# Optimization experiments

Hardware: AMD Instinct MI355X
Metric: run time of the kernel (lower is better)

The kernel has to match this reference:

```python
import jax, jax.numpy as jnp
import numpy as np

N = 50000      # total nodes in batch
E = 600000     # total edges
F_IN = 128     # num_features
H = 128        # nhid
C = 10         # num_classes
G = 100        # number of graphs in batch
RATIO = 0.5    # pooling_ratio


def _glorot(k, shape):
    lim = (6.0 / (shape[0] + shape[1])) ** 0.5
    return jax.random.uniform(k, shape, minval=-lim, maxval=lim, dtype=jnp.float32)


def setup_inputs() -> dict:
    key = jax.random.key(0)
    ks = jax.random.split(key, 20)
    inp = {
        "x": jax.random.normal(ks[0], (N, F_IN), dtype=jnp.float32),
        "edge_index": jax.random.randint(ks[1], (2, E), 0, N),
        "batch": jnp.sort(jax.random.randint(ks[2], (N,), 0, G)),
        # conv1/pool1
        "W1": _glorot(ks[3], (F_IN, H)), "b1": jnp.zeros((H,), jnp.float32),
        "Ws1": _glorot(ks[4], (H, 1)), "bs1": jnp.zeros((1,), jnp.float32),
        # conv2/pool2
        "W2": _glorot(ks[5], (H, H)), "b2": jnp.zeros((H,), jnp.float32),
        "Ws2": _glorot(ks[6], (H, 1)), "bs2": jnp.zeros((1,), jnp.float32),
        # conv3/pool3
        "W3": _glorot(ks[7], (H, H)), "b3": jnp.zeros((H,), jnp.float32),
        "Ws3": _glorot(ks[8], (H, 1)), "bs3": jnp.zeros((1,), jnp.float32),
        # MLP head
        "Wl1": _glorot(ks[9], (2 * H, H)), "bl1": jnp.zeros((H,), jnp.float32),
        "Wl2": _glorot(ks[10], (H, H // 2)), "bl2": jnp.zeros((H // 2,), jnp.float32),
        "Wl3": _glorot(ks[11], (H // 2, C)), "bl3": jnp.zeros((C,), jnp.float32),
    }
    return inp


def _gcn_conv(x, W, b, src, dst, ew):
    # PyG GCNConv: D^{-1/2}(A+I)D^{-1/2} X W + b, with masked edge weights ew.
    xw = x @ W                                                  # [N, out]
    deg = jax.ops.segment_sum(ew, dst, num_segments=N) + 1.0    # self-loop
    norm = jax.lax.rsqrt(deg)
    coef = norm[src] * norm[dst] * ew                           # [E]
    agg = jax.ops.segment_sum(xw[src] * coef[:, None], dst, num_segments=N)
    return agg + xw * (norm * norm)[:, None] + b


def _topk_mask(score, node_mask, batch, ratio):
    # Per-graph top-ceil(ratio * active) selection, expressed as a node mask.
    score_m = jnp.where(node_mask > 0, score, -jnp.inf)
    active = jax.ops.segment_sum(node_mask, batch, num_segments=G)
    k = jnp.ceil(ratio * active)
    order = jnp.argsort(-score_m)                         # score desc
    perm = order[jnp.argsort(batch[order], stable=True)]  # batch asc, score desc
    total = jax.ops.segment_sum(jnp.ones((N,), score.dtype), batch, num_segments=G)
    starts = jnp.cumsum(total) - total
    b_sorted = batch[perm]
    rank = jnp.arange(N, dtype=score.dtype) - starts[b_sorted]
    keep_sorted = rank < k[b_sorted]
    keep = jnp.zeros((N,), bool).at[perm].set(keep_sorted)
    return node_mask * keep.astype(node_mask.dtype)


def _readout(x, node_mask, batch):
    # [gmp | gap] per graph, honoring the active-node mask.
    m = node_mask[:, None]
    s = jax.ops.segment_sum(x * m, batch, num_segments=G)
    cnt = jax.ops.segment_sum(node_mask, batch, num_segments=G)
    mean = s / jnp.maximum(cnt, 1.0)[:, None]
    xm = jnp.where(m > 0, x, -jnp.inf)
    mx = jax.ops.segment_max(xm, batch, num_segments=G)
    mx = jnp.where(jnp.isfinite(mx), mx, 0.0)
    return jnp.concatenate([mx, mean], axis=1)            # [G, 2H]


def reference(x, edge_index, batch, W1, b1, Ws1, bs1, W2, b2, Ws2, bs2,
              W3, b3, Ws3, bs3, Wl1, bl1, Wl2, bl2, Wl3, bl3):
    src, dst = edge_index[0], edge_index[1]

    def block(h, mask, W, b, Ws, bs):
        ew = mask[src] * mask[dst]
        h = jax.nn.relu(_gcn_conv(h, W, b, src, dst, ew))
        score = _gcn_conv(h, Ws, bs, src, dst, ew)[:, 0]
        new_mask = _topk_mask(score, mask, batch, RATIO)
        h = h * jnp.tanh(score)[:, None] * new_mask[:, None]
        return h, new_mask

    mask = jnp.ones((N,), jnp.float32)
    h, mask = block(x, mask, W1, b1, Ws1, bs1)
    r1 = _readout(h, mask, batch)
    h, mask = block(h, mask, W2, b2, Ws2, bs2)
    r2 = _readout(h, mask, batch)
    h, mask = block(h, mask, W3, b3, Ws3, bs3)
    r3 = _readout(h, mask, batch)

    z = r1 + r2 + r3                                       # [G, 2H]
    z = jax.nn.relu(z @ Wl1 + bl1)                         # dropout is eval-mode no-op
    z = jax.nn.relu(z @ Wl2 + bl2)
    return jax.nn.log_softmax(z @ Wl3 + bl3, axis=-1)      # [G, C]
```

## Files before the change

### kernel.cpp

```cpp
#include <hip/hip_runtime.h>
#include <math.h>

#define N_NODES 50000
#define N_EDGES 600000
#define H 128
#define G_GRAPHS 100
#define C_CLS 10
#define NBLK_SCAN ((N_NODES + 255) / 256)
#define RSUB 16


__global__ void fill_kernel(float* __restrict__ p, float v, int n) {
    int i = blockIdx.x * 256 + threadIdx.x;
    if (i < n) p[i] = v;
}

__global__ void starts_kernel(const int* __restrict__ batch, int* __restrict__ starts, int n) {
    int i = blockIdx.x * 256 + threadIdx.x;
    if (i >= n) return;
    int b = batch[i];
    int prev = (i == 0) ? -1 : batch[i - 1];
    for (int g = prev + 1; g <= b; ++g) starts[g] = i;
    if (i == n - 1) {
        for (int g = b + 1; g < G_GRAPHS; ++g) starts[g] = n;
    }
}

__global__ void counts_kernel(const int* __restrict__ starts, int* __restrict__ counts) {
    int g = threadIdx.x;
    if (g < G_GRAPHS) {
        int e = (g == G_GRAPHS - 1) ? N_NODES : starts[g + 1];
        counts[g] = e - starts[g];
    }
}


__global__ void indeg_kernel(const int* __restrict__ dst, int* __restrict__ indeg, int ne) {
    int e = blockIdx.x * 256 + threadIdx.x;
    if (e < ne) atomicAdd(&indeg[dst[e]], 1);
}

__global__ void bsum_kernel(const int* __restrict__ indeg, int* __restrict__ bsum, int n) {
    __shared__ int red[256];
    int i = blockIdx.x * 256 + threadIdx.x;
    red[threadIdx.x] = (i < n) ? indeg[i] : 0;
    __syncthreads();
    for (int o = 128; o > 0; o >>= 1) {
        if (threadIdx.x < o) red[threadIdx.x] += red[threadIdx.x + o];
        __syncthreads();
    }
    if (threadIdx.x == 0) bsum[blockIdx.x] = red[0];
}

__global__ void bscan_kernel(const int* __restrict__ bsum, int* __restrict__ boff, int nb) {
    __shared__ int s[256];
    int t = threadIdx.x;
    s[t] = (t < nb) ? bsum[t] : 0;
    __syncthreads();
    for (int o = 1; o < 256; o <<= 1) {
        int v = (t >= o) ? s[t - o] : 0;
        __syncthreads();
        s[t] += v;
        __syncthreads();
    }
    if (t < nb) boff[t] = (t == 0) ? 0 : s[t - 1];
}

__global__ void rowptr_kernel(const int* __restrict__ indeg, const int* __restrict__ boff,
                              int* __restrict__ rowptr, int n) {
    __shared__ int s[256];
    int i = blockIdx.x * 256 + threadIdx.x;
    int t = threadIdx.x;
    int v = (i < n) ? indeg[i] : 0;
    s[t] = v;
    __syncthreads();
    for (int o = 1; o < 256; o <<= 1) {
        int u = (t >= o) ? s[t - o] : 0;
        __syncthreads();
        s[t] += u;
        __syncthreads();
    }
    int incl = s[t];
    int excl = incl - v;
    if (i < n) rowptr[i] = boff[blockIdx.x] + excl;
    if (i == n - 1) rowptr[n] = boff[blockIdx.x] + incl;
}

__global__ void scatter_kernel(const int* __restrict__ src, const int* __restrict__ dst,
                               const int* __restrict__ rowptr, int* __restrict__ cursor,
                               int* __restrict__ srcC, int ne) {
    int e = blockIdx.x * 256 + threadIdx.x;
    if (e >= ne) return;
    int d = dst[e];
    int pos = rowptr[d] + atomicAdd(&cursor[d], 1);
    srcC[pos] = src[e];
}


__global__ __launch_bounds__(256) void wsort_kernel(const int* __restrict__ rowptr,
                                                    int* __restrict__ srcC, int n) {
    int node = blockIdx.x * 4 + (threadIdx.x >> 6);
    if (node >= n) return;
    int lane = threadIdx.x & 63;
    int e0 = rowptr[node], e1 = rowptr[node + 1];
    int len = e1 - e0;
    if (len <= 1) return;
    if (len <= 64) {
        int key = (lane < len) ? srcC[e0 + lane] : 0x7fffffff;
        for (int p = 0; p < len; ++p) {
            int partner = ((lane ^ p) & 1) ? lane - 1 : lane + 1;
            int pv = __shfl(key, partner & 63, 64);
            if (partner >= 0 && partner < 64) {
                key = (partner > lane) ? min(key, pv) : max(key, pv);
            }
        }
        if (lane < len) srcC[e0 + lane] = key;
    } else {
        if (lane == 0) {
            for (int i = e0 + 1; i < e1; ++i) {
                int k = srcC[i];
                int j = i - 1;
                while (j >= e0 && srcC[j] > k) { srcC[j + 1] = srcC[j]; --j; }
                srcC[j + 1] = k;
            }
        }
    }
}


__global__ void degnorm_kernel(const int* __restrict__ rowptr, const int* __restrict__ srcC,
                               const float* __restrict__ mask, float* __restrict__ norm,
                               float* __restrict__ mnorm, int n) {
    int idx = blockIdx.x * 256 + threadIdx.x;
    int d = idx >> 3;
    if (d >= n) return;
    int l = idx & 7;
    float md = mask[d];
    float s = 0.f;
    if (md != 0.f) {
        int e0 = rowptr[d], e1 = rowptr[d + 1];
        for (int e = e0 + l; e < e1; e += 8) s += mask[srcC[e]];
    }
#pragma unroll
    for (int o = 4; o > 0; o >>= 1) s += __shfl_down(s, o, 8);
    if (l == 0) {
        float nd = rsqrtf(1.f + md * s);
        norm[d] = nd;
        mnorm[d] = md * nd;
    }
}


__global__ __launch_bounds__(256) void gemm128_kernel(const float* __restrict__ A,
                                                      const float* __restrict__ W,
                                                      const float* __restrict__ gf,
                                                      float* __restrict__ out, int nrows) {
    __shared__ float sT[128][68];
    int row0 = blockIdx.x * 64;
    int tid = threadIdx.x;
    for (int i = tid; i < 2048; i += 256) {
        int r = i >> 5, c4 = i & 31;
        int row = row0 + r;
        float4 v = make_float4(0.f, 0.f, 0.f, 0.f);
        if (row < nrows) {
            float g = gf[row];
            v = ((const float4*)(A + (size_t)row * H))[c4];
            v.x *= g; v.y *= g; v.z *= g; v.w *= g;
        }
        sT[c4 * 4 + 0][r] = v.x; sT[c4 * 4 + 1][r] = v.y;
        sT[c4 * 4 + 2][r] = v.z; sT[c4 * 4 + 3][r] = v.w;
    }
    __syncthreads();
    int cg = tid & 31;
    int rg = tid >> 5;
    float acc[8][4];
#pragma unroll
    for (int i = 0; i < 8; ++i)
#pragma unroll
        for (int j = 0; j < 4; ++j) acc[i][j] = 0.f;

#pragma unroll 4
    for (int k = 0; k < 128; ++k) {
        float4 w4 = ((const float4*)(W + k * H))[cg];
        const float4* pa = (const float4*)(&sT[k][rg * 8]);
        float4 a0 = pa[0], a1 = pa[1];
        float av[8] = {a0.x, a0.y, a0.z, a0.w, a1.x, a1.y, a1.z, a1.w};
#pragma unroll
        for (int i = 0; i < 8; ++i) {
            acc[i][0] = fmaf(av[i], w4.x, acc[i][0]);
            acc[i][1] = fmaf(av[i], w4.y, acc[i][1]);
            acc[i][2] = fmaf(av[i], w4.z, acc[i][2]);
            acc[i][3] = fmaf(av[i], w4.w, acc[i][3]);
        }
    }
#pragma unroll
    for (int i = 0; i < 8; ++i) {
        int row = row0 + rg * 8 + i;
        if (row < nrows) {
            float4 o = make_float4(acc[i][0], acc[i][1], acc[i][2], acc[i][3]);
            ((float4*)(out + (size_t)row * H))[cg] = o;
        }
    }
}


__global__ __launch_bounds__(256) void agg_fused_kernel(const float* __restrict__ xw,
        const int* __restrict__ rowptr, const int* __restrict__ srcC,
        const float* __restrict__ mask, const float* __restrict__ norm,
        const float* __restrict__ mnorm,
        const float* __restrict__ b, const float* __restrict__ Ws,
        float* __restrict__ hout, float* __restrict__ xws, int n) {
    int node = blockIdx.x * 8 + (threadIdx.x >> 5);
    if (node >= n) return;
    int t = threadIdx.x & 31;
    const float4* xw4 = (const float4*)xw;
    float md = mask[node];
    float nd = norm[node];
    float4 a0 = make_float4(0.f, 0.f, 0.f, 0.f);
    float4 a1 = a0, a2 = a0, a3 = a0;
    if (md != 0.f) {
        int e0 = rowptr[node], e1 = rowptr[node + 1];
        int e = e0;
        for (; e + 3 < e1; e += 4) {
            int s0 = srcC[e], s1 = srcC[e + 1], s2 = srcC[e + 2], s3 = srcC[e + 3];
            float c0 = mnorm[s0];
            float c1 = mnorm[s1];
            float c2 = mnorm[s2];
            float c3 = mnorm[s3];
            if (c0 != 0.f) {
                float4 v = xw4[(size_t)s0 * 32 + t];
                a0.x = fmaf(v.x, c0, a0.x); a0.y = fmaf(v.y, c0, a0.y);
                a0.z = fmaf(v.z, c0, a0.z); a0.w = fmaf(v.w, c0, a0.w);
            }
            if (c1 != 0.f) {
                float4 v = xw4[(size_t)s1 * 32 + t];
                a1.x = fmaf(v.x, c1, a1.x); a1.y = fmaf(v.y, c1, a1.y);
                a1.z = fmaf(v.z, c1, a1.z); a1.w = fmaf(v.w, c1, a1.w);
            }
            if (c2 != 0.f) {
                float4 v = xw4[(size_t)s2 * 32 + t];
                a2.x = fmaf(v.x, c2, a2.x); a2.y = fmaf(v.y, c2, a2.y);
                a2.z = fmaf(v.z, c2, a2.z); a2.w = fmaf(v.w, c2, a2.w);
            }
            if (c3 != 0.f) {
                float4 v = xw4[(size_t)s3 * 32 + t];
                a3.x = fmaf(v.x, c3, a3.x); a3.y = fmaf(v.y, c3, a3.y);
                a3.z = fmaf(v.z, c3, a3.z); a3.w = fmaf(v.w, c3, a3.w);
            }
        }
        for (; e < e1; ++e) {
            int s = srcC[e];
            float c = mnorm[s];
            if (c != 0.f) {
                float4 v = xw4[(size_t)s * 32 + t];
                a0.x = fmaf(v.x, c, a0.x); a0.y = fmaf(v.y, c, a0.y);
                a0.z = fmaf(v.z, c, a0.z); a0.w = fmaf(v.w, c, a0.w);
            }
        }
        float sc = md * nd;
        a0.x = (((a0.x + a1.x) + a2.x) + a3.x) * sc;
        a0.y = (((a0.y + a1.y) + a2.y) + a3.y) * sc;
        a0.z = (((a0.z + a1.z) + a2.z) + a3.z) * sc;
        a0.w = (((a0.w + a1.w) + a2.w) + a3.w) * sc;
    }
    float4 self = xw4[(size_t)node * 32 + t];
    float4 bb = ((const float4*)b)[t];
    float n2 = nd * nd;
    float4 v;
    v.x = fmaxf(fmaf(self.x, n2, a0.x) + bb.x, 0.f);
    v.y = fmaxf(fmaf(self.y, n2, a0.y) + bb.y, 0.f);
    v.z = fmaxf(fmaf(self.z, n2, a0.z) + bb.z, 0.f);
    v.w = fmaxf(fmaf(self.w, n2, a0.w) + bb.w, 0.f);
    ((float4*)hout)[(size_t)node * 32 + t] = v;
    float4 w = ((const float4*)Ws)[t];
    float p = ((v.x * w.x + v.y * w.y) + v.z * w.z) + v.w * w.w;
#pragma unroll
    for (int o = 16; o > 0; o >>= 1) p += __shfl_down(p, o, 32);
    if (t == 0) xws[node] = p;
}


__global__ void score_gather_kernel(const int* __restrict__ rowptr, const int* __restrict__ srcC,
        const float* __restrict__ xws, const float* __restrict__ mask,
        const float* __restrict__ norm, const float* __restrict__ mnorm,
        const float* __restrict__ bs, float* __restrict__ scorem, int n) {
    int idx = blockIdx.x * 256 + threadIdx.x;
    int d = idx >> 3;
    if (d >= n) return;
    int l = idx & 7;
    float md = mask[d];
    float nd = norm[d];
    float acc = 0.f;
    if (md != 0.f) {
        int e0 = rowptr[d], e1 = rowptr[d + 1];
        for (int e = e0 + l; e < e1; e += 8) {
            int s = srcC[e];
            acc = fmaf(xws[s], mnorm[s], acc);
        }
    }
#pragma unroll
    for (int o = 4; o > 0; o >>= 1) acc += __shfl_down(acc, o, 8);
    if (l == 0) {
        float out;
        if (md != 0.f) out = acc * (md * nd) + xws[d] * nd * nd + bs[0];
        else out = -INFINITY;
        scorem[d] = out;
    }
}


__global__ __launch_bounds__(256) void kk_kernel(const float* __restrict__ scorem,
        const int* __restrict__ starts, const int* __restrict__ counts,
        int* __restrict__ kkarr) {
    int g = blockIdx.x;
    int s0 = starts[g], cnt = counts[g];
    __shared__ int red[256];
    int c = 0;
    for (int i = threadIdx.x; i < cnt; i += 256)
        if (scorem[s0 + i] != -INFINITY) ++c;
    red[threadIdx.x] = c;
    __syncthreads();
    for (int o = 128; o > 0; o >>= 1) {
        if (threadIdx.x < o) red[threadIdx.x] += red[threadIdx.x + o];
        __syncthreads();
    }
    if (threadIdx.x == 0) kkarr[g] = (int)ceilf(0.5f * (float)red[0]);
}


__global__ __launch_bounds__(256) void rank_kernel(const float* __restrict__ scorem,
        const float* __restrict__ mask, const int* __restrict__ batch,
        const int* __restrict__ starts, const int* __restrict__ counts,
        const int* __restrict__ kkarr,
        float* __restrict__ nmask, float* __restrict__ gfac, int n) {
    int i = blockIdx.x * 4 + (threadIdx.x >> 6);
    if (i >= n) return;
    int lane = threadIdx.x & 63;
    float sci = scorem[i];
    if (sci == -INFINITY) {
        if (lane == 0) { nmask[i] = 0.f; gfac[i] = 0.f; }
        return;
    }
    int g = batch[i];
    int s0 = starts[g], cnt = counts[g];
    int r = 0;
    for (int j = lane; j < cnt; j += 64) {
        float sj = scorem[s0 + j];
        if (sj > sci || (sj == sci && (s0 + j) < i)) ++r;
    }
#pragma unroll
    for (int o = 32; o > 0; o >>= 1) r += __shfl_down(r, o);
    if (lane == 0) {
        bool keep = (r < kkarr[g]);
        float m = mask[i];
        nmask[i] = keep ? m : 0.f;
        gfac[i] = keep ? tanhf(sci) * m : 0.f;
    }
}


__global__ __launch_bounds__(128) void readout_part_kernel(const float* __restrict__ h,
        const float* __restrict__ mask, const float* __restrict__ gfac,
        const int* __restrict__ starts, const int* __restrict__ counts,
        float* __restrict__ partS, float* __restrict__ partM, float* __restrict__ partC) {
    int g = blockIdx.x >> 4;
    int sub = blockIdx.x & (RSUB - 1);
    int f = threadIdx.x;
    int s0 = starts[g], cnt = counts[g];
    float s = 0.f, mx = -INFINITY, c = 0.f;
    for (int i = sub; i < cnt; i += RSUB) {
        float m = mask[s0 + i];
        if (m > 0.f) {
            float v = h[(size_t)(s0 + i) * H + f] * gfac[s0 + i];
            s += v; mx = fmaxf(mx, v); c += 1.f;
        }
    }
    size_t pidx = (size_t)blockIdx.x * H + f;
    partS[pidx] = s;
    partM[pidx] = mx;
    if (f == 0) partC[blockIdx.x] = c;
}


__global__ __launch_bounds__(128) void readout_comb_kernel(const float* __restrict__ partS,
        const float* __restrict__ partM, const float* __restrict__ partC,
        float* __restrict__ r) {
    int g = blockIdx.x;
    int f = threadIdx.x;
    float S = 0.f, M = -INFINITY, C = 0.f;
    for (int sub = 0; sub < RSUB; ++sub) {
        size_t pidx = (size_t)(g * RSUB + sub) * H + f;
        S += partS[pidx];
        M = fmaxf(M, partM[pidx]);
        C += partC[g * RSUB + sub];
    }
    float mean = S / fmaxf(C, 1.f);
    if (C == 0.f) M = 0.f;
    r[(size_t)g * 2 * H + f] += M;
    r[(size_t)g * 2 * H + H + f] += mean;
}


__global__ __launch_bounds__(128) void mlp_kernel(const float* __restrict__ r,
        const float* __restrict__ Wl1, const float* __restrict__ bl1,
        const float* __restrict__ Wl2, const float* __restrict__ bl2,
        const float* __restrict__ Wl3, const float* __restrict__ bl3,
        float* __restrict__ out) {
    int g = blockIdx.x;
    int t = threadIdx.x;
    __shared__ float sz[256];
    __shared__ float sy1[128];
    __shared__ float sy2[64];
    __shared__ float sy3[10];
    __shared__ float sred[2];
    sz[t] = r[g * 256 + t];
    sz[t + 128] = r[g * 256 + 128 + t];
    __syncthreads();
    float a = bl1[t];
    for (int k = 0; k < 256; ++k) a = fmaf(sz[k], Wl1[k * 128 + t], a);
    sy1[t] = fmaxf(a, 0.f);
    __syncthreads();
    if (t < 64) {
        float a2 = bl2[t];
        for (int k = 0; k < 128; ++k) a2 = fmaf(sy1[k], Wl2[k * 64 + t], a2);
        sy2[t] = fmaxf(a2, 0.f);
    }
    __syncthreads();
    if (t < 10) {
        float a3 = bl3[t];
        for (int k = 0; k < 64; ++k) a3 = fmaf(sy2[k], Wl3[k * 10 + t], a3);
        sy3[t] = a3;
    }
    __syncthreads();
    if (t == 0) {
        float m = sy3[0];
        for (int c2 = 1; c2 < 10; ++c2) m = fmaxf(m, sy3[c2]);
        float se = 0.f;
        for (int c2 = 0; c2 < 10; ++c2) se += expf(sy3[c2] - m);
        sred[0] = m; sred[1] = logf(se);
    }
    __syncthreads();
    if (t < 10) out[g * 10 + t] = sy3[t] - sred[0] - sred[1];
}


extern "C" void kernel_launch(void* const* d_in, const int* in_sizes, int n_in,
                              void* d_out, int out_size, void* d_ws, size_t ws_size,
                              hipStream_t stream) {
    const float* x     = (const float*)d_in[0];
    const int*   ei    = (const int*)d_in[1];
    const int*   batch = (const int*)d_in[2];
    const int* src  = ei;
    const int* dstp = ei + N_EDGES;
    const float* Wb[3]  = {(const float*)d_in[3], (const float*)d_in[7],  (const float*)d_in[11]};
    const float* bbv[3] = {(const float*)d_in[4], (const float*)d_in[8],  (const float*)d_in[12]};
    const float* Wsb[3] = {(const float*)d_in[5], (const float*)d_in[9],  (const float*)d_in[13]};
    const float* bsb[3] = {(const float*)d_in[6], (const float*)d_in[10], (const float*)d_in[14]};
    const float* Wl1 = (const float*)d_in[15];
    const float* bl1 = (const float*)d_in[16];
    const float* Wl2 = (const float*)d_in[17];
    const float* bl2 = (const float*)d_in[18];
    const float* Wl3 = (const float*)d_in[19];
    const float* bl3 = (const float*)d_in[20];
    float* out = (float*)d_out;

    float* fws = (float*)d_ws;
    size_t off = 0;
    float* hA     = fws + off; off += (size_t)N_NODES * H;
    float* hB     = fws + off; off += (size_t)N_NODES * H;
    float* xw     = fws + off; off += (size_t)N_NODES * H;
    float* scorem = fws + off; off += N_NODES;
    float* xws    = fws + off; off += N_NODES;
    float* norm   = fws + off; off += N_NODES;
    float* mnorm  = fws + off; off += N_NODES;
    float* mA     = fws + off; off += N_NODES;
    float* mB     = fws + off; off += N_NODES;
    float* gfac   = fws + off; off += N_NODES;
    float* rbuf   = fws + off; off += (size_t)G_GRAPHS * 2 * H;
    float* partS  = fws + off; off += (size_t)G_GRAPHS * RSUB * H;
    float* partM  = fws + off; off += (size_t)G_GRAPHS * RSUB * H;
    float* partC  = fws + off; off += (size_t)G_GRAPHS * RSUB;
    int* counts   = (int*)(fws + off); off += G_GRAPHS;
    int* starts   = (int*)(fws + off); off += G_GRAPHS;
    int* kkarr    = (int*)(fws + off); off += G_GRAPHS;
    int* rowptr   = (int*)(fws + off); off += N_NODES + 1;
    int* indeg    = (int*)(fws + off); off += N_NODES;
    int* cursor   = (int*)(fws + off); off += N_NODES;
    int* bsum     = (int*)(fws + off); off += NBLK_SCAN;
    int* boff     = (int*)(fws + off); off += NBLK_SCAN;
    int* srcC     = (int*)(fws + off); off += N_EDGES;

    int nblkN  = (N_NODES + 255) / 256;
    int nblkN8 = (N_NODES * 8 + 255) / 256;
    int nblkE  = (N_EDGES + 255) / 256;

    starts_kernel<<<nblkN, 256, 0, stream>>>(batch, starts, N_NODES);
    counts_kernel<<<1, 128, 0, stream>>>(starts, counts);

    hipMemsetAsync(indeg, 0, N_NODES * sizeof(int), stream);
    hipMemsetAsync(cursor, 0, N_NODES * sizeof(int), stream);
    indeg_kernel<<<nblkE, 256, 0, stream>>>(dstp, indeg, N_EDGES);
    bsum_kernel<<<NBLK_SCAN, 256, 0, stream>>>(indeg, bsum, N_NODES);
    bscan_kernel<<<1, 256, 0, stream>>>(bsum, boff, NBLK_SCAN);
    rowptr_kernel<<<NBLK_SCAN, 256, 0, stream>>>(indeg, boff, rowptr, N_NODES);
    scatter_kernel<<<nblkE, 256, 0, stream>>>(src, dstp, rowptr, cursor, srcC, N_EDGES);
    wsort_kernel<<<(N_NODES + 3) / 4, 256, 0, stream>>>(rowptr, srcC, N_NODES);

    fill_kernel<<<nblkN, 256, 0, stream>>>(mA, 1.f, N_NODES);
    fill_kernel<<<nblkN, 256, 0, stream>>>(gfac, 1.f, N_NODES);
    hipMemsetAsync(rbuf, 0, G_GRAPHS * 2 * H * sizeof(float), stream);

    const float* hin = x;
    float* hout = hA;
    const float* mcur = mA;
    float* mnext = mB;

    for (int blk = 0; blk < 3; ++blk) {
        degnorm_kernel<<<nblkN8, 256, 0, stream>>>(rowptr, srcC, mcur, norm, mnorm, N_NODES);
        gemm128_kernel<<<(N_NODES + 63) / 64, 256, 0, stream>>>(hin, Wb[blk], gfac, xw, N_NODES);
        agg_fused_kernel<<<(N_NODES + 7) / 8, 256, 0, stream>>>(xw, rowptr, srcC, mcur, norm,
                                                                mnorm, bbv[blk], Wsb[blk],
                                                                hout, xws, N_NODES);
        score_gather_kernel<<<nblkN8, 256, 0, stream>>>(rowptr, srcC, xws, mcur, norm, mnorm,
                                                        bsb[blk], scorem, N_NODES);
        kk_kernel<<<G_GRAPHS, 256, 0, stream>>>(scorem, starts, counts, kkarr);
        rank_kernel<<<(N_NODES + 3) / 4, 256, 0, stream>>>(scorem, mcur, batch, starts, counts,
                                                           kkarr, mnext, gfac, N_NODES);
        readout_part_kernel<<<G_GRAPHS * RSUB, 128, 0, stream>>>(hout, mnext, gfac, starts,
                                                                 counts, partS, partM, partC);
        readout_comb_kernel<<<G_GRAPHS, 128, 0, stream>>>(partS, partM, partC, rbuf);
        hin = hout;
        hout = (hout == hA) ? hB : hA;
        const float* tm = mcur; mcur = mnext; mnext = (float*)tm;
    }

    mlp_kernel<<<G_GRAPHS, 128, 0, stream>>>(rbuf, Wl1, bl1, Wl2, bl2, Wl3, bl3, out);
}
```

Baseline: 458.7 us.

## Compact active nodes for pooled-layer GEMMs and fold k computation into rank

After each pooling step, the surviving nodes are compacted into an index list with an atomic counter. Later blocks then run the transform GEMM only on active rows, which should roughly halve and then quarter that work. The separate kk kernel is removed by counting active scores inside rank_kernel, and the first block's aggregation drops its zero-coefficient branch. In exchange this adds a compaction kernel, a memset, indirect row loads, and a GEMM grid sized for all nodes in which most blocks exit early. Rows left uncomputed in xw are stale, but their aggregation coefficients are zero, so the guarded path never reads them.

```diff
diff --git a/kernel.cpp b/kernel.cpp
--- a/kernel.cpp
+++ b/kernel.cpp
@@ -151,6 +151,16 @@
 }
 
 
+__global__ void compact_kernel(const float* __restrict__ nmask, int* __restrict__ alist,
+                               int* __restrict__ alcnt, int n) {
+    int i = blockIdx.x * 256 + threadIdx.x;
+    if (i < n && nmask[i] > 0.f) {
+        int pos = atomicAdd(alcnt, 1);
+        alist[pos] = i;
+    }
+}
+
+
 __global__ __launch_bounds__(256) void gemm128_kernel(const float* __restrict__ A,
                                                       const float* __restrict__ W,
                                                       const float* __restrict__ gf,
@@ -204,6 +214,67 @@
 }
 
 
+__global__ __launch_bounds__(256) void gemm128c_kernel(const float* __restrict__ A,
+                                                       const float* __restrict__ W,
+                                                       const float* __restrict__ gf,
+                                                       const int* __restrict__ alist,
+                                                       const int* __restrict__ alcnt,
+                                                       float* __restrict__ out) {
+    int nact = *alcnt;
+    int row0 = blockIdx.x * 64;
+    if (row0 >= nact) return;
+    __shared__ float sT[128][68];
+    __shared__ int ridx[64];
+    int tid = threadIdx.x;
+    if (tid < 64) ridx[tid] = (row0 + tid < nact) ? alist[row0 + tid] : -1;
+    __syncthreads();
+    for (int i = tid; i < 2048; i += 256) {
+        int r = i >> 5, c4 = i & 31;
+        int row = ridx[r];
+        float4 v = make_float4(0.f, 0.f, 0.f, 0.f);
+        if (row >= 0) {
+            float g = gf[row];
+            v = ((const float4*)(A + (size_t)row * H))[c4];
+            v.x *= g; v.y *= g; v.z *= g; v.w *= g;
+        }
+        sT[c4 * 4 + 0][r] = v.x; sT[c4 * 4 + 1][r] = v.y;
+        sT[c4 * 4 + 2][r] = v.z; sT[c4 * 4 + 3][r] = v.w;
+    }
+    __syncthreads();
+    int cg = tid & 31;
+    int rg = tid >> 5;
+    float acc[8][4];
+#pragma unroll
+    for (int i = 0; i < 8; ++i)
+#pragma unroll
+        for (int j = 0; j < 4; ++j) acc[i][j] = 0.f;
+
+#pragma unroll 4
+    for (int k = 0; k < 128; ++k) {
+        float4 w4 = ((const float4*)(W + k * H))[cg];
+        const float4* pa = (const float4*)(&sT[k][rg * 8]);
+        float4 a0 = pa[0], a1 = pa[1];
+        float av[8] = {a0.x, a0.y, a0.z, a0.w, a1.x, a1.y, a1.z, a1.w};
+#pragma unroll
+        for (int i = 0; i < 8; ++i) {
+            acc[i][0] = fmaf(av[i], w4.x, acc[i][0]);
+            acc[i][1] = fmaf(av[i], w4.y, acc[i][1]);
+            acc[i][2] = fmaf(av[i], w4.z, acc[i][2]);
+            acc[i][3] = fmaf(av[i], w4.w, acc[i][3]);
+        }
+    }
+#pragma unroll
+    for (int i = 0; i < 8; ++i) {
+        int row = ridx[rg * 8 + i];
+        if (row >= 0) {
+            float4 o = make_float4(acc[i][0], acc[i][1], acc[i][2], acc[i][3]);
+            ((float4*)(out + (size_t)row * H))[cg] = o;
+        }
+    }
+}
+
+
+template <bool GUARD>
 __global__ __launch_bounds__(256) void agg_fused_kernel(const float* __restrict__ xw,
         const int* __restrict__ rowptr, const int* __restrict__ srcC,
         const float* __restrict__ mask, const float* __restrict__ norm,
@@ -227,22 +298,22 @@
             float c1 = mnorm[s1];
             float c2 = mnorm[s2];
             float c3 = mnorm[s3];
-            if (c0 != 0.f) {
+            if (!GUARD || c0 != 0.f) {
                 float4 v = xw4[(size_t)s0 * 32 + t];
                 a0.x = fmaf(v.x, c0, a0.x); a0.y = fmaf(v.y, c0, a0.y);
                 a0.z = fmaf(v.z, c0, a0.z); a0.w = fmaf(v.w, c0, a0.w);
             }
-            if (c1 != 0.f) {
+            if (!GUARD || c1 != 0.f) {
                 float4 v = xw4[(size_t)s1 * 32 + t];
                 a1.x = fmaf(v.x, c1, a1.x); a1.y = fmaf(v.y, c1, a1.y);
                 a1.z = fmaf(v.z, c1, a1.z); a1.w = fmaf(v.w, c1, a1.w);
             }
-            if (c2 != 0.f) {
+            if (!GUARD || c2 != 0.f) {
                 float4 v = xw4[(size_t)s2 * 32 + t];
                 a2.x = fmaf(v.x, c2, a2.x); a2.y = fmaf(v.y, c2, a2.y);
                 a2.z = fmaf(v.z, c2, a2.z); a2.w = fmaf(v.w, c2, a2.w);
             }
-            if (c3 != 0.f) {
+            if (!GUARD || c3 != 0.f) {
                 float4 v = xw4[(size_t)s3 * 32 + t];
                 a3.x = fmaf(v.x, c3, a3.x); a3.y = fmaf(v.y, c3, a3.y);
                 a3.z = fmaf(v.z, c3, a3.z); a3.w = fmaf(v.w, c3, a3.w);
@@ -251,7 +322,7 @@
         for (; e < e1; ++e) {
             int s = srcC[e];
             float c = mnorm[s];
-            if (c != 0.f) {
+            if (!GUARD || c != 0.f) {
                 float4 v = xw4[(size_t)s * 32 + t];
                 a0.x = fmaf(v.x, c, a0.x); a0.y = fmaf(v.y, c, a0.y);
                 a0.z = fmaf(v.z, c, a0.z); a0.w = fmaf(v.w, c, a0.w);
@@ -295,7 +366,8 @@
         int e0 = rowptr[d], e1 = rowptr[d + 1];
         for (int e = e0 + l; e < e1; e += 8) {
             int s = srcC[e];
-            acc = fmaf(xws[s], mnorm[s], acc);
+            float c = mnorm[s];
+            if (c != 0.f) acc = fmaf(xws[s], c, acc);
         }
     }
 #pragma unroll
@@ -309,29 +381,9 @@
 }
 
 
-__global__ __launch_bounds__(256) void kk_kernel(const float* __restrict__ scorem,
-        const int* __restrict__ starts, const int* __restrict__ counts,
-        int* __restrict__ kkarr) {
-    int g = blockIdx.x;
-    int s0 = starts[g], cnt = counts[g];
-    __shared__ int red[256];
-    int c = 0;
-    for (int i = threadIdx.x; i < cnt; i += 256)
-        if (scorem[s0 + i] != -INFINITY) ++c;
-    red[threadIdx.x] = c;
-    __syncthreads();
-    for (int o = 128; o > 0; o >>= 1) {
-        if (threadIdx.x < o) red[threadIdx.x] += red[threadIdx.x + o];
-        __syncthreads();
-    }
-    if (threadIdx.x == 0) kkarr[g] = (int)ceilf(0.5f * (float)red[0]);
-}
-
-
 __global__ __launch_bounds__(256) void rank_kernel(const float* __restrict__ scorem,
         const float* __restrict__ mask, const int* __restrict__ batch,
         const int* __restrict__ starts, const int* __restrict__ counts,
-        const int* __restrict__ kkarr,
         float* __restrict__ nmask, float* __restrict__ gfac, int n) {
     int i = blockIdx.x * 4 + (threadIdx.x >> 6);
     if (i >= n) return;
@@ -343,15 +395,22 @@
     }
     int g = batch[i];
     int s0 = starts[g], cnt = counts[g];
-    int r = 0;
+    int r = 0, act = 0;
     for (int j = lane; j < cnt; j += 64) {
         float sj = scorem[s0 + j];
-        if (sj > sci || (sj == sci && (s0 + j) < i)) ++r;
-    }
-#pragma unroll
-    for (int o = 32; o > 0; o >>= 1) r += __shfl_down(r, o);
+        if (sj != -INFINITY) {
+            ++act;
+            if (sj > sci || (sj == sci && (s0 + j) < i)) ++r;
+        }
+    }
+#pragma unroll
+    for (int o = 32; o > 0; o >>= 1) {
+        r += __shfl_down(r, o);
+        act += __shfl_down(act, o);
+    }
     if (lane == 0) {
-        bool keep = (r < kkarr[g]);
+        int kk = (int)ceilf(0.5f * (float)act);
+        bool keep = (r < kk);
         float m = mask[i];
         nmask[i] = keep ? m : 0.f;
         gfac[i] = keep ? tanhf(sci) * m : 0.f;
@@ -482,17 +541,19 @@
     float* partC  = fws + off; off += (size_t)G_GRAPHS * RSUB;
     int* counts   = (int*)(fws + off); off += G_GRAPHS;
     int* starts   = (int*)(fws + off); off += G_GRAPHS;
-    int* kkarr    = (int*)(fws + off); off += G_GRAPHS;
     int* rowptr   = (int*)(fws + off); off += N_NODES + 1;
     int* indeg    = (int*)(fws + off); off += N_NODES;
     int* cursor   = (int*)(fws + off); off += N_NODES;
     int* bsum     = (int*)(fws + off); off += NBLK_SCAN;
     int* boff     = (int*)(fws + off); off += NBLK_SCAN;
+    int* alist    = (int*)(fws + off); off += N_NODES;
+    int* alcnt    = (int*)(fws + off); off += 1;
     int* srcC     = (int*)(fws + off); off += N_EDGES;
 
     int nblkN  = (N_NODES + 255) / 256;
     int nblkN8 = (N_NODES * 8 + 255) / 256;
     int nblkE  = (N_EDGES + 255) / 256;
+    int nblkG  = (N_NODES + 63) / 64;
 
     starts_kernel<<<nblkN, 256, 0, stream>>>(batch, starts, N_NODES);
     counts_kernel<<<1, 128, 0, stream>>>(starts, counts);
@@ -517,15 +578,23 @@
 
     for (int blk = 0; blk < 3; ++blk) {
         degnorm_kernel<<<nblkN8, 256, 0, stream>>>(rowptr, srcC, mcur, norm, mnorm, N_NODES);
-        gemm128_kernel<<<(N_NODES + 63) / 64, 256, 0, stream>>>(hin, Wb[blk], gfac, xw, N_NODES);
-        agg_fused_kernel<<<(N_NODES + 7) / 8, 256, 0, stream>>>(xw, rowptr, srcC, mcur, norm,
-                                                                mnorm, bbv[blk], Wsb[blk],
-                                                                hout, xws, N_NODES);
+        if (blk == 0) {
+            gemm128_kernel<<<nblkG, 256, 0, stream>>>(hin, Wb[blk], gfac, xw, N_NODES);
+            agg_fused_kernel<false><<<(N_NODES + 7) / 8, 256, 0, stream>>>(
+                xw, rowptr, srcC, mcur, norm, mnorm, bbv[blk], Wsb[blk], hout, xws, N_NODES);
+        } else {
+            gemm128c_kernel<<<nblkG, 256, 0, stream>>>(hin, Wb[blk], gfac, alist, alcnt, xw);
+            agg_fused_kernel<true><<<(N_NODES + 7) / 8, 256, 0, stream>>>(
+                xw, rowptr, srcC, mcur, norm, mnorm, bbv[blk], Wsb[blk], hout, xws, N_NODES);
+        }
         score_gather_kernel<<<nblkN8, 256, 0, stream>>>(rowptr, srcC, xws, mcur, norm, mnorm,
                                                         bsb[blk], scorem, N_NODES);
-        kk_kernel<<<G_GRAPHS, 256, 0, stream>>>(scorem, starts, counts, kkarr);
         rank_kernel<<<(N_NODES + 3) / 4, 256, 0, stream>>>(scorem, mcur, batch, starts, counts,
-                                                           kkarr, mnext, gfac, N_NODES);
+                                                           mnext, gfac, N_NODES);
+        if (blk < 2) {
+            hipMemsetAsync(alcnt, 0, sizeof(int), stream);
+            compact_kernel<<<nblkN, 256, 0, stream>>>(mnext, alist, alcnt, N_NODES);
+        }
         readout_part_kernel<<<G_GRAPHS * RSUB, 128, 0, stream>>>(hout, mnext, gfac, starts,
                                                                  counts, partS, partM, partC);
         readout_comb_kernel<<<G_GRAPHS, 128, 0, stream>>>(partS, partM, partC, rbuf);
```

Result: no change. 451.2 us (-1.6%).
